# Kernel tuning notes

Hardware: AMD Instinct MI355X
Metric: run time of the kernel (lower is better)

Reference implementation:

```python
import jax, jax.numpy as jnp
import numpy as np

K = 4            # mhc_expansion_rate (n streams)
B = 2            # batch
S = 1024         # sequence length
D = 1024         # emb_dim
EPS = 1e-6       # RMSNorm epsilon
SINKHORN_ITERS = 20
SINKHORN_SCALING = 0.05
RES_ALPHA_SCALE = 1e-4
PRE_ALPHA_SCALE = 1e-4
POST_ALPHA_SCALE = 1e-4


def setup_inputs() -> dict:
    key = jax.random.key(0)
    ks = jax.random.split(key, 4)
    return {
        "x": jax.random.normal(ks[0], (K, B, S, D), dtype=jnp.float32),
        "norm_weight": jnp.ones((D,), dtype=jnp.float32),
        "res_alpha": jax.random.normal(ks[1], (K, B, S, D, K * K), dtype=jnp.float32),
        "pre_alpha": jax.random.normal(ks[2], (K, B, S, D, K), dtype=jnp.float32),
        "post_alpha": jax.random.normal(ks[3], (K, B, S, D, K), dtype=jnp.float32),
        "res_beta": jnp.zeros((K,), dtype=jnp.float32),
        "pre_beta": jnp.zeros((K,), dtype=jnp.float32),
        "post_beta": jnp.zeros((K,), dtype=jnp.float32),
    }


def rms_norm(x, weight):
    # normalize over the last (emb) dim
    var = jnp.mean(jnp.square(x), axis=-1, keepdims=True)
    return x * jax.lax.rsqrt(var + EPS) * weight


def sinkhorn_log(logits, iterations=SINKHORN_ITERS, scaling=SINKHORN_SCALING):
    # log-domain Sinkhorn -> doubly stochastic (k,k) matrix
    Z = logits / scaling
    log_marginal = jnp.zeros((logits.shape[-1],), dtype=logits.dtype)

    def body_fn(i, state):
        u, v = state
        u = log_marginal - jax.scipy.special.logsumexp(Z + v[None, :], axis=-1)
        v = log_marginal - jax.scipy.special.logsumexp(Z + u[:, None], axis=-2)
        return (u, v)

    u0 = jnp.zeros(logits.shape[:-1], dtype=logits.dtype)
    v0 = jnp.zeros(logits.shape[:-1], dtype=logits.dtype)
    u, v = jax.lax.fori_loop(0, iterations, body_fn, (u0, v0))
    return jnp.exp(Z + u[:, None] + v[None, :])


def _mapping(x, alpha_scale, alpha, beta, scale):
    h = jnp.einsum('nbsd,nbsdm->m', x, alpha)   # full-tensor reduce -> (m,)
    return scale * jax.nn.sigmoid(alpha_scale * h + beta)


def reference(x, norm_weight, res_alpha, pre_alpha, post_alpha,
              res_beta, pre_beta, post_beta):
    xn = rms_norm(x, norm_weight)                                   # (n,b,s,d)

    pre_mapping = _mapping(xn, PRE_ALPHA_SCALE, pre_alpha, pre_beta, 1.0)   # (k,)
    layer_input = jnp.einsum('nbsd,n->bsd', xn, pre_mapping)        # (b,s,d)

    layer_out = layer_input  # branch_fn == identity for the reference

    post_mapping = _mapping(xn, POST_ALPHA_SCALE, post_alpha, post_beta, 2.0)  # (k,)
    post_out = jnp.einsum('bsd,n->nbsd', layer_out, post_mapping)   # (n,b,s,d)

    h_res = jnp.einsum('nbsd,nbsdm->m', xn, res_alpha).reshape(K, K)
    res_map = sinkhorn_log(RES_ALPHA_SCALE * h_res + res_beta)      # (k,k)
    res_out = jnp.einsum('nbsd,nm->mbsd', xn, res_map)              # (k,b,s,d)

    return (res_out, post_out)
```

## Files before the change

### kernel.cpp

```cpp
#include <hip/hip_runtime.h>
#include <math.h>

#define KK 4
#define BB 2
#define SS 1024
#define DD 1024
#define EPSV 1e-6f
#define BSD   (BB*SS*DD)
#define NBSD  (KK*BB*SS*DD)
#define ROWS  (KK*BB*SS)
#define NSLOTS 64
#define NACC 24

#define ACC_N (NSLOTS*NACC)

__global__ __launch_bounds__(256) void k1_reduce(const float* __restrict__ x,
                                                 const float* __restrict__ w,
                                                 const float* __restrict__ res_a,
                                                 const float* __restrict__ pre_a,
                                                 const float* __restrict__ post_a,
                                                 float* __restrict__ ws_acc,
                                                 float* __restrict__ ws_inv) {
    const int row  = blockIdx.x;
    const int t    = threadIdx.x;
    const int wave = t >> 6, lane = t & 63;

    float4 xv = ((const float4*)(x + (size_t)row * DD))[t];
    float ss = xv.x*xv.x + xv.y*xv.y + xv.z*xv.z + xv.w*xv.w;
    #pragma unroll
    for (int o = 32; o > 0; o >>= 1) ss += __shfl_down(ss, o, 64);

    __shared__ float s_ss[4];
    if (lane == 0) s_ss[wave] = ss;
    __syncthreads();
    float inv = rsqrtf((s_ss[0] + s_ss[1] + s_ss[2] + s_ss[3]) * (1.0f / (float)DD) + EPSV);
    if (t == 0) ws_inv[row] = inv;

    float4 wv = ((const float4*)w)[t];
    float xn[4] = { xv.x*inv*wv.x, xv.y*inv*wv.y, xv.z*inv*wv.z, xv.w*inv*wv.w };

    float acc[NACC];
    #pragma unroll
    for (int j = 0; j < NACC; j++) acc[j] = 0.f;

    const size_t base = (size_t)row * DD + (size_t)t * 4;
    const float4* ra = (const float4*)(res_a  + base * 16);
    const float4* pa = (const float4*)(pre_a  + base * 4);
    const float4* qa = (const float4*)(post_a + base * 4);

    #pragma unroll
    for (int j = 0; j < 4; j++) {
        const float xnj = xn[j];
        #pragma unroll
        for (int q = 0; q < 4; q++) {
            float4 a = ra[j*4 + q];
            acc[q*4+0] += xnj * a.x;
            acc[q*4+1] += xnj * a.y;
            acc[q*4+2] += xnj * a.z;
            acc[q*4+3] += xnj * a.w;
        }
        float4 p = pa[j];
        acc[16] += xnj * p.x; acc[17] += xnj * p.y;
        acc[18] += xnj * p.z; acc[19] += xnj * p.w;
        float4 q4 = qa[j];
        acc[20] += xnj * q4.x; acc[21] += xnj * q4.y;
        acc[22] += xnj * q4.z; acc[23] += xnj * q4.w;
    }

    #pragma unroll
    for (int j = 0; j < NACC; j++) {
        #pragma unroll
        for (int o = 32; o > 0; o >>= 1) acc[j] += __shfl_down(acc[j], o, 64);
    }
    __shared__ float s_acc[4][NACC];
    if (lane == 0) {
        #pragma unroll
        for (int j = 0; j < NACC; j++) s_acc[wave][j] = acc[j];
    }
    __syncthreads();
    if (t < NACC) {
        float v = s_acc[0][t] + s_acc[1][t] + s_acc[2][t] + s_acc[3][t];
        atomicAdd(&ws_acc[(blockIdx.x & (NSLOTS-1)) * NACC + t], v);
    }
}

__global__ void k2_maps(const float* __restrict__ ws_acc,
                        const float* __restrict__ res_beta,
                        const float* __restrict__ pre_beta,
                        const float* __restrict__ post_beta,
                        float* __restrict__ maps) {
    if (threadIdx.x != 0 || blockIdx.x != 0) return;
    float h[NACC];
    for (int j = 0; j < NACC; j++) {
        float s = 0.f;
        for (int sl = 0; sl < NSLOTS; sl++) s += ws_acc[sl*NACC + j];
        h[j] = s;
    }
    for (int i = 0; i < 4; i++) {
        float hp = 1e-4f * h[16+i] + pre_beta[i];
        maps[i]     = 1.f / (1.f + expf(-hp));
        float hq = 1e-4f * h[20+i] + post_beta[i];
        maps[4+i]   = 2.f / (1.f + expf(-hq));
    }
    float Z[4][4];
    for (int i = 0; i < 4; i++)
        for (int j = 0; j < 4; j++)
            Z[i][j] = (1e-4f * h[i*4 + j] + res_beta[j]) * (1.0f / 0.05f);
    float u[4] = {0,0,0,0}, v[4] = {0,0,0,0};
    for (int it = 0; it < 20; it++) {
        for (int i = 0; i < 4; i++) {
            float m = Z[i][0]+v[0];
            for (int j = 1; j < 4; j++) { float tt = Z[i][j]+v[j]; m = tt > m ? tt : m; }
            float s = 0.f;
            for (int j = 0; j < 4; j++) s += expf(Z[i][j]+v[j]-m);
            u[i] = -(m + logf(s));
        }
        for (int j = 0; j < 4; j++) {
            float m = Z[0][j]+u[0];
            for (int i = 1; i < 4; i++) { float tt = Z[i][j]+u[i]; m = tt > m ? tt : m; }
            float s = 0.f;
            for (int i = 0; i < 4; i++) s += expf(Z[i][j]+u[i]-m);
            v[j] = -(m + logf(s));
        }
    }
    for (int i = 0; i < 4; i++)
        for (int j = 0; j < 4; j++)
            maps[8 + i*4 + j] = expf(Z[i][j] + u[i] + v[j]);
}

__global__ __launch_bounds__(256) void k3_out(const float* __restrict__ x,
                                              const float* __restrict__ w,
                                              const float* __restrict__ ws_inv,
                                              const float* __restrict__ maps,
                                              float* __restrict__ out) {
    const int tid = blockIdx.x * 256 + threadIdx.x;
    const size_t e = (size_t)tid * 4;
    const int bs = (int)(e >> 10);

    float pre_m[4], post_m[4], rm[16];
    #pragma unroll
    for (int i = 0; i < 4; i++)  { pre_m[i] = maps[i]; post_m[i] = maps[4+i]; }
    #pragma unroll
    for (int i = 0; i < 16; i++) rm[i] = maps[8+i];

    float4 wv = *(const float4*)(w + (e & (DD-1)));

    float li_x = 0.f, li_y = 0.f, li_z = 0.f, li_w = 0.f;
    float4 res[4];
    #pragma unroll
    for (int m = 0; m < 4; m++) res[m] = make_float4(0.f, 0.f, 0.f, 0.f);

    #pragma unroll
    for (int n = 0; n < 4; n++) {
        const float iv = ws_inv[n * (BB*SS) + bs];
        float4 xv = *(const float4*)(x + (size_t)n * BSD + e);
        float xnx = xv.x * iv * wv.x;
        float xny = xv.y * iv * wv.y;
        float xnz = xv.z * iv * wv.z;
        float xnw = xv.w * iv * wv.w;
        const float pm = pre_m[n];
        li_x += xnx * pm; li_y += xny * pm; li_z += xnz * pm; li_w += xnw * pm;
        #pragma unroll
        for (int m = 0; m < 4; m++) {
            const float r = rm[n*4 + m];
            res[m].x += xnx * r; res[m].y += xny * r;
            res[m].z += xnz * r; res[m].w += xnw * r;
        }
    }
    #pragma unroll
    for (int m = 0; m < 4; m++)
        *(float4*)(out + (size_t)m * BSD + e) = res[m];
    #pragma unroll
    for (int n = 0; n < 4; n++) {
        const float pm = post_m[n];
        *(float4*)(out + (size_t)NBSD + (size_t)n * BSD + e) =
            make_float4(li_x * pm, li_y * pm, li_z * pm, li_w * pm);
    }
}

extern "C" void kernel_launch(void* const* d_in, const int* in_sizes, int n_in,
                              void* d_out, int out_size, void* d_ws, size_t ws_size,
                              hipStream_t stream) {
    const float* x      = (const float*)d_in[0];
    const float* w      = (const float*)d_in[1];
    const float* res_a  = (const float*)d_in[2];
    const float* pre_a  = (const float*)d_in[3];
    const float* post_a = (const float*)d_in[4];
    const float* res_b  = (const float*)d_in[5];
    const float* pre_b  = (const float*)d_in[6];
    const float* post_b = (const float*)d_in[7];

    float* ws      = (float*)d_ws;
    float* ws_acc  = ws;
    float* ws_inv  = ws + ACC_N;
    float* ws_maps = ws + ACC_N + ROWS;

    hipMemsetAsync(ws_acc, 0, NSLOTS * NACC * sizeof(float), stream);

    k1_reduce<<<ROWS, 256, 0, stream>>>(x, w, res_a, pre_a, post_a, ws_acc, ws_inv);
    k2_maps<<<1, 64, 0, stream>>>(ws_acc, res_b, pre_b, post_b, ws_maps);
    k3_out<<<BSD/1024, 256, 0, stream>>>(x, w, ws_inv, ws_maps, (float*)d_out);
}
```

Baseline: 1.012 ms.

## Coalesce alpha loads in reduce kernel by staging normalized row in LDS

The normalized row is now written to shared memory, so each thread can read consecutive float4 chunks of res_alpha, pre_alpha and post_alpha with a stride across threads (c*256+t). Before, each thread walked its own contiguous 64-float span, which makes the wave's loads strided. Each thread now keeps only 4+4+4 partial sums instead of 24, which cuts the shuffle reduction work and register use. The cost is an extra LDS round trip and an extra barrier per block.

```diff
diff --git a/kernel.cpp b/kernel.cpp
--- a/kernel.cpp
+++ b/kernel.cpp
@@ -11,7 +11,6 @@
 #define ROWS  (KK*BB*SS)
 #define NSLOTS 64
 #define NACC 24
-
 #define ACC_N (NSLOTS*NACC)
 
 __global__ __launch_bounds__(256) void k1_reduce(const float* __restrict__ x,
@@ -25,62 +24,70 @@
     const int t    = threadIdx.x;
     const int wave = t >> 6, lane = t & 63;
 
+    __shared__ float s_xn[DD];
+    __shared__ float s_ss[4];
+
     float4 xv = ((const float4*)(x + (size_t)row * DD))[t];
     float ss = xv.x*xv.x + xv.y*xv.y + xv.z*xv.z + xv.w*xv.w;
     #pragma unroll
     for (int o = 32; o > 0; o >>= 1) ss += __shfl_down(ss, o, 64);
-
-    __shared__ float s_ss[4];
     if (lane == 0) s_ss[wave] = ss;
     __syncthreads();
     float inv = rsqrtf((s_ss[0] + s_ss[1] + s_ss[2] + s_ss[3]) * (1.0f / (float)DD) + EPSV);
     if (t == 0) ws_inv[row] = inv;
 
     float4 wv = ((const float4*)w)[t];
-    float xn[4] = { xv.x*inv*wv.x, xv.y*inv*wv.y, xv.z*inv*wv.z, xv.w*inv*wv.w };
-
-    float acc[NACC];
-    #pragma unroll
-    for (int j = 0; j < NACC; j++) acc[j] = 0.f;
-
-    const size_t base = (size_t)row * DD + (size_t)t * 4;
-    const float4* ra = (const float4*)(res_a  + base * 16);
-    const float4* pa = (const float4*)(pre_a  + base * 4);
-    const float4* qa = (const float4*)(post_a + base * 4);
+    ((float4*)s_xn)[t] = make_float4(xv.x*inv*wv.x, xv.y*inv*wv.y,
+                                     xv.z*inv*wv.z, xv.w*inv*wv.w);
+    __syncthreads();
+
+    float ar[4] = {0.f, 0.f, 0.f, 0.f};
+    const float4* ra = (const float4*)(res_a + (size_t)row * DD * 16);
+    #pragma unroll
+    for (int c = 0; c < 16; c++) {
+        float4 a = ra[c * 256 + t];
+        float xs = s_xn[c * 64 + (t >> 2)];
+        ar[0] += xs * a.x; ar[1] += xs * a.y;
+        ar[2] += xs * a.z; ar[3] += xs * a.w;
+    }
+
+    float ap[4] = {0.f,0.f,0.f,0.f}, aq[4] = {0.f,0.f,0.f,0.f};
+    const float4* pa = (const float4*)(pre_a  + (size_t)row * DD * 4);
+    const float4* qa = (const float4*)(post_a + (size_t)row * DD * 4);
+    #pragma unroll
+    for (int c = 0; c < 4; c++) {
+        float xs = s_xn[c * 256 + t];
+        float4 p = pa[c * 256 + t];
+        ap[0] += xs * p.x; ap[1] += xs * p.y;
+        ap[2] += xs * p.z; ap[3] += xs * p.w;
+        float4 q = qa[c * 256 + t];
+        aq[0] += xs * q.x; aq[1] += xs * q.y;
+        aq[2] += xs * q.z; aq[3] += xs * q.w;
+    }
 
     #pragma unroll
     for (int j = 0; j < 4; j++) {
-        const float xnj = xn[j];
-        #pragma unroll
-        for (int q = 0; q < 4; q++) {
-            float4 a = ra[j*4 + q];
-            acc[q*4+0] += xnj * a.x;
-            acc[q*4+1] += xnj * a.y;
-            acc[q*4+2] += xnj * a.z;
-            acc[q*4+3] += xnj * a.w;
-        }
-        float4 p = pa[j];
-        acc[16] += xnj * p.x; acc[17] += xnj * p.y;
-        acc[18] += xnj * p.z; acc[19] += xnj * p.w;
-        float4 q4 = qa[j];
-        acc[20] += xnj * q4.x; acc[21] += xnj * q4.y;
-        acc[22] += xnj * q4.z; acc[23] += xnj * q4.w;
-    }
-
-    #pragma unroll
-    for (int j = 0; j < NACC; j++) {
-        #pragma unroll
-        for (int o = 32; o > 0; o >>= 1) acc[j] += __shfl_down(acc[j], o, 64);
-    }
-    __shared__ float s_acc[4][NACC];
+        #pragma unroll
+        for (int o = 32; o >= 4; o >>= 1) ar[j] += __shfl_down(ar[j], o, 64);
+        #pragma unroll
+        for (int o = 32; o >= 1; o >>= 1) {
+            ap[j] += __shfl_down(ap[j], o, 64);
+            aq[j] += __shfl_down(aq[j], o, 64);
+        }
+    }
+    __shared__ float s_red[4][NACC];
+    if (lane < 4) {
+        #pragma unroll
+        for (int j = 0; j < 4; j++) s_red[wave][lane*4 + j] = ar[j];
+    }
     if (lane == 0) {
         #pragma unroll
-        for (int j = 0; j < NACC; j++) s_acc[wave][j] = acc[j];
+        for (int j = 0; j < 4; j++) { s_red[wave][16 + j] = ap[j]; s_red[wave][20 + j] = aq[j]; }
     }
     __syncthreads();
     if (t < NACC) {
-        float v = s_acc[0][t] + s_acc[1][t] + s_acc[2][t] + s_acc[3][t];
-        atomicAdd(&ws_acc[(blockIdx.x & (NSLOTS-1)) * NACC + t], v);
+        float v = s_red[0][t] + s_red[1][t] + s_red[2][t] + s_red[3][t];
+        atomicAdd(&ws_acc[(row & (NSLOTS-1)) * NACC + t], v);
     }
 }
 
```

New measurement: 930.2 us. 8.1% less time.
